# Performance work log

Measured on AMD Instinct MI355X. Metric: run time of the kernel, lower is better.

Reference implementation:

```python
import jax, jax.numpy as jnp
import numpy as np

B, S, D = 2, 2048, 2048
H, DK, DV, L = 16, 128, 128, 64


def setup_inputs() -> dict:
    key = jax.random.key(0)
    ks = jax.random.split(key, 12)
    s = lambda k, shape, fan_in: jax.random.normal(k, shape, jnp.float32) / np.sqrt(fan_in)
    return {
        "queries": jax.random.normal(ks[0], (B, S, D), jnp.float32),
        "keys": jax.random.normal(ks[1], (B, S, D), jnp.float32),
        "values": jax.random.normal(ks[2], (B, S, D), jnp.float32),
        "Wq": s(ks[3], (D, H * DK), D), "bq": jnp.zeros((H * DK,), jnp.float32),
        "Wlk": s(ks[4], (D, H * L), D), "blk": jnp.zeros((H * L,), jnp.float32),
        "Wlv": s(ks[5], (D, H * L), D), "blv": jnp.zeros((H * L,), jnp.float32),
        "Wkr": s(ks[6], (L, DK), L),
        "Wvr": s(ks[7], (L, DV), L),
        "Wout": s(ks[8], (H * DV, D), H * DV), "bout": jnp.zeros((D,), jnp.float32),
    }


def reference(queries, keys, values, Wq, bq, Wlk, blk, Wlv, blv, Wkr, Wvr, Wout, bout):
    b, sq, _ = queries.shape
    sk = keys.shape[1]
    # projections -> [b, h, s, d]
    q = (queries @ Wq + bq).reshape(b, sq, H, DK).transpose(0, 2, 1, 3)
    lk = (keys @ Wlk + blk).reshape(b, sk, H, L).transpose(0, 2, 1, 3)
    lv = (values @ Wlv + blv).reshape(b, sk, H, L).transpose(0, 2, 1, 3)
    k = lk @ Wkr  # [b,h,sk,DK] latent -> key reconstruction
    v = lv @ Wvr  # [b,h,sk,DV]
    scores = jnp.einsum('bhqd,bhkd->bhqk', q, k) / np.sqrt(DK).astype(np.float32)
    causal = jnp.triu(jnp.ones((sq, sk), dtype=bool), k=1)
    scores = jnp.where(causal, -jnp.inf, scores)
    attn = jax.nn.softmax(scores, axis=-1)
    out = jnp.einsum('bhqk,bhkd->bhqd', attn, v)
    out = out.transpose(0, 2, 1, 3).reshape(b, sq, H * DV)
    return out @ Wout + bout
```

## Files before the change

### kernel.cpp

```cpp
#include <hip/hip_runtime.h>
#include <cstdint>
#include <cstddef>

typedef _Float16 f16;
typedef __attribute__((ext_vector_type(8))) _Float16 f16x8;
typedef __attribute__((ext_vector_type(4))) _Float16 f16x4;
typedef __attribute__((ext_vector_type(4))) float f32x4;

constexpr int kB  = 2;
constexpr int kS  = 2048;
constexpr int kD  = 2048;
constexpr int kH  = 16;
constexpr int kL  = 64;
constexpr int kHL = kH * kL;
constexpr int kBS = kB * kS;

__device__ __forceinline__ void load_lds16(const void* g, void* l) {
  __builtin_amdgcn_global_load_lds((const __attribute__((address_space(1))) void*)g,
                                   (__attribute__((address_space(3))) void*)l, 16, 0, 0);
}

__device__ __forceinline__ f32x4 mfma16(f16x8 a, f16x8 b, f32x4 c) {
  return __builtin_amdgcn_mfma_f32_16x16x32_f16(a, b, c, 0, 0, 0);
}


__global__ void cast4(const float* __restrict__ a, const float* __restrict__ b,
                      const float* __restrict__ c, const float* __restrict__ d,
                      f16* __restrict__ oa, f16* __restrict__ ob,
                      f16* __restrict__ oc, f16* __restrict__ od) {
  const int z = blockIdx.z;
  int i = blockIdx.x * 256 + threadIdx.x;
  if (z == 3 && i >= kD * kD / 4) return;
  const float* in = z == 0 ? a : z == 1 ? b : z == 2 ? c : d;
  f16* out = z == 0 ? oa : z == 1 ? ob : z == 2 ? oc : od;
  float4 f = ((const float4*)in)[i];
  f16x4 o; o[0] = (f16)f.x; o[1] = (f16)f.y; o[2] = (f16)f.z; o[3] = (f16)f.w;
  ((f16x4*)out)[i] = o;
}

__device__ __forceinline__ void transpose_body(const float* __restrict__ in,
                                               f16* __restrict__ out, int R, int C) {
  const int r0 = blockIdx.y * 64, c0 = blockIdx.x * 64;
  __shared__ float tile[64][65];
  const int t = threadIdx.x;
  const int cc = t & 63, rr = t >> 6;
#pragma unroll
  for (int p = 0; p < 16; p++) {
    int r = p * 4 + rr;
    tile[r][cc] = in[(size_t)(r0 + r) * C + c0 + cc];
  }
  __syncthreads();
#pragma unroll
  for (int p = 0; p < 16; p++) {
    int c = p * 4 + rr;
    out[(size_t)(c0 + c) * R + r0 + cc] = (f16)tile[cc][c];
  }
}

__global__ __launch_bounds__(256) void transpose3(const float* __restrict__ Wlk,
                                                  const float* __restrict__ Wlv,
                                                  const float* __restrict__ Wout,
                                                  f16* __restrict__ Wlkt,
                                                  f16* __restrict__ Wlvt,
                                                  f16* __restrict__ WoutT) {
  const int z = blockIdx.z;
  if (z < 2 && blockIdx.x >= 16) return;
  if (z == 0) transpose_body(Wlk, Wlkt, 2048, 1024);
  else if (z == 1) transpose_body(Wlv, Wlvt, 2048, 1024);
  else transpose_body(Wout, WoutT, 2048, 2048);
}

__global__ void fold_bq(const float* __restrict__ bq, const float* __restrict__ Wkr,
                        float* __restrict__ bql) {
  int hl = blockIdx.x * 256 + threadIdx.x;
  if (hl >= kHL) return;
  int h = hl >> 6, l = hl & 63;
  float s = 0.f;
  for (int c = 0; c < 128; c++) s += bq[h * 128 + c] * Wkr[l * 128 + c];
  bql[hl] = s;
}

__global__ __launch_bounds__(256) void fold2(const float* __restrict__ Wkr,
                                             const float* __restrict__ Wvr,
                                             const f16* __restrict__ Wq16,
                                             const f16* __restrict__ WoutT,
                                             f16* __restrict__ Wqlt,
                                             f16* __restrict__ W2t) {
  __shared__ f16 sA[64 * 136];
  __shared__ f16 sB[128 * 128];
  const int z = blockIdx.z;
  const int h = blockIdx.y;
  const int d0 = blockIdx.x * 128;
  const float* Wsm = z ? Wvr : Wkr;
  const f16* Bsrc = (z ? WoutT : Wq16) + h * 128;
  const int tid = threadIdx.x;
  const int w = tid >> 6, lane = tid & 63;
  const int quad = lane >> 4, l16 = lane & 15;

#pragma unroll
  for (int it = 0; it < 8; it++) {
    int i = it * 256 + tid;
    float4 f = ((const float4*)Wsm)[i];
    int e = i * 4, r = e >> 7, c = e & 127;
    f16x4 o; o[0] = (f16)f.x; o[1] = (f16)f.y; o[2] = (f16)f.z; o[3] = (f16)f.w;
    *(f16x4*)&sA[r * 136 + c] = o;
  }
#pragma unroll
  for (int c = 0; c < 8; c++) {
    int rbase = w * 32 + c * 4;
    load_lds16(Bsrc + (size_t)(d0 + rbase + (lane >> 4)) * 2048 + (lane & 15) * 8,
               &sB[rbase * 128]);
  }
  __syncthreads();

  if (z == 0) {
    f32x4 acc[4][2];
    for (int mt = 0; mt < 4; mt++)
      for (int nt = 0; nt < 2; nt++) acc[mt][nt] = (f32x4){0.f, 0.f, 0.f, 0.f};
#pragma unroll
    for (int ks = 0; ks < 4; ks++) {
      f16x8 af[4], bf[2];
#pragma unroll
      for (int mt = 0; mt < 4; mt++)
        af[mt] = *(const f16x8*)&sA[(mt * 16 + l16) * 136 + ks * 32 + quad * 8];
#pragma unroll
      for (int nt = 0; nt < 2; nt++)
        bf[nt] = *(const f16x8*)&sB[(w * 32 + nt * 16 + l16) * 128 + ks * 32 + quad * 8];
#pragma unroll
      for (int mt = 0; mt < 4; mt++)
#pragma unroll
        for (int nt = 0; nt < 2; nt++) acc[mt][nt] = mfma16(af[mt], bf[nt], acc[mt][nt]);
    }
#pragma unroll
    for (int mt = 0; mt < 4; mt++)
#pragma unroll
      for (int nt = 0; nt < 2; nt++)
#pragma unroll
        for (int r = 0; r < 4; r++) {
          int row = mt * 16 + quad * 4 + r;
          int col = d0 + w * 32 + nt * 16 + l16;
          Wqlt[(size_t)(h * 64 + row) * 2048 + col] = (f16)acc[mt][nt][r];
        }
  } else {
    f32x4 acc[2][4];
    for (int mt = 0; mt < 2; mt++)
      for (int nt = 0; nt < 4; nt++) acc[mt][nt] = (f32x4){0.f, 0.f, 0.f, 0.f};
#pragma unroll
    for (int ks = 0; ks < 4; ks++) {
      f16x8 af[2], bf[4];
#pragma unroll
      for (int mt = 0; mt < 2; mt++)
        af[mt] = *(const f16x8*)&sB[(w * 32 + mt * 16 + l16) * 128 + ks * 32 + quad * 8];
#pragma unroll
      for (int nt = 0; nt < 4; nt++)
        bf[nt] = *(const f16x8*)&sA[(nt * 16 + l16) * 136 + ks * 32 + quad * 8];
#pragma unroll
      for (int mt = 0; mt < 2; mt++)
#pragma unroll
        for (int nt = 0; nt < 4; nt++) acc[mt][nt] = mfma16(af[mt], bf[nt], acc[mt][nt]);
    }
#pragma unroll
    for (int mt = 0; mt < 2; mt++)
#pragma unroll
      for (int nt = 0; nt < 4; nt++)
#pragma unroll
        for (int r = 0; r < 4; r++) {
          int row = d0 + w * 32 + mt * 16 + quad * 4 + r;
          int col = nt * 16 + l16;
          W2t[(size_t)row * 1024 + h * 64 + col] = (f16)acc[mt][nt][r];
        }
  }
}

template <typename OutT, bool HAS_BIAS>
__device__ __forceinline__ void gemm_body(const f16* __restrict__ A, const f16* __restrict__ Bt,
                                          const float* __restrict__ bias, OutT* __restrict__ C,
                                          int N, int K) {
  __shared__ f16 sA[128 * 64];
  __shared__ f16 sB[128 * 64];
  const int tid = threadIdx.x;
  const int w = tid >> 6, lane = tid & 63;
  const int quad = lane >> 4, l16 = lane & 15;
  const int wm = w >> 1, wn = w & 1;
  const int m0 = blockIdx.y * 128, n0 = blockIdx.x * 128;
  const int rowA = lane >> 3;
  const int colSw = (((lane & 7) ^ (lane >> 3)) << 3) ;
  const int sw0 = ((quad ^ (l16 & 7)) << 3);
  const int sw1 = (((4 + quad) ^ (l16 & 7)) << 3);

  f32x4 acc[4][4];
  for (int i = 0; i < 4; i++)
    for (int j = 0; j < 4; j++) acc[i][j] = (f32x4){0.f, 0.f, 0.f, 0.f};

  for (int k0 = 0; k0 < K; k0 += 64) {
    __syncthreads();
#pragma unroll
    for (int c = 0; c < 4; c++) {
      int rl = w * 32 + c * 8;
      load_lds16(A + (size_t)(m0 + rl + rowA) * K + k0 + colSw, &sA[rl * 64]);
      load_lds16(Bt + (size_t)(n0 + rl + rowA) * K + k0 + colSw, &sB[rl * 64]);
    }
    __syncthreads();
#pragma unroll
    for (int ks = 0; ks < 2; ks++) {
      const int sw = ks ? sw1 : sw0;
      f16x8 af[4], bfr[4];
#pragma unroll
      for (int mt = 0; mt < 4; mt++)
        af[mt] = *(const f16x8*)&sA[(wm * 64 + mt * 16 + l16) * 64 + sw];
#pragma unroll
      for (int nt = 0; nt < 4; nt++)
        bfr[nt] = *(const f16x8*)&sB[(wn * 64 + nt * 16 + l16) * 64 + sw];
#pragma unroll
      for (int mt = 0; mt < 4; mt++) {
#pragma unroll
        for (int nt = 0; nt < 4; nt++)
          acc[mt][nt] = mfma16(af[mt], bfr[nt], acc[mt][nt]);
      }
    }
  }
#pragma unroll
  for (int mt = 0; mt < 4; mt++) {
#pragma unroll
    for (int nt = 0; nt < 4; nt++) {
      int col = n0 + wn * 64 + nt * 16 + l16;
      float bv = HAS_BIAS ? bias[col] : 0.f;
#pragma unroll
      for (int r = 0; r < 4; r++) {
        int row = m0 + wm * 64 + mt * 16 + quad * 4 + r;
        C[(size_t)row * N + col] = (OutT)(acc[mt][nt][r] + bv);
      }
    }
  }
}

__global__ __launch_bounds__(256) void gemm3_f16(
    const f16* __restrict__ A0, const f16* __restrict__ A1, const f16* __restrict__ A2,
    const f16* __restrict__ B0, const f16* __restrict__ B1, const f16* __restrict__ B2,
    const float* __restrict__ c0, const float* __restrict__ c1, const float* __restrict__ c2,
    f16* __restrict__ C0, f16* __restrict__ C1, f16* __restrict__ C2, int N, int K) {
  const f16* A = blockIdx.z == 0 ? A0 : blockIdx.z == 1 ? A1 : A2;
  const f16* Bt = blockIdx.z == 0 ? B0 : blockIdx.z == 1 ? B1 : B2;
  const float* bias = blockIdx.z == 0 ? c0 : blockIdx.z == 1 ? c1 : c2;
  f16* C = blockIdx.z == 0 ? C0 : blockIdx.z == 1 ? C1 : C2;
  gemm_body<f16, true>(A, Bt, bias, C, N, K);
}

__global__ __launch_bounds__(256) void gemm_f32(const f16* __restrict__ A,
                                                const f16* __restrict__ Bt,
                                                const float* __restrict__ bias,
                                                float* __restrict__ C, int N, int K) {
  gemm_body<float, true>(A, Bt, bias, C, N, K);
}

__global__ __launch_bounds__(256) void transpose_lv(const f16* __restrict__ LV,
                                                    f16* __restrict__ LVt) {
  const int bh = blockIdx.y, b = bh >> 4, h = bh & 15;
  const int s0 = blockIdx.x * 64;
  __shared__ f16 tile[64][65];
  const int t = threadIdx.x;
  const int c0 = t & 63, r0 = t >> 6;
#pragma unroll
  for (int r = 0; r < 16; r++) {
    int s = r * 4 + r0;
    tile[s][c0] = LV[(size_t)(b * kS + s0 + s) * kHL + h * kL + c0];
  }
  __syncthreads();
#pragma unroll
  for (int r = 0; r < 16; r++) {
    int vl = r * 4 + r0;
    LVt[((size_t)bh * kL + vl) * kS + s0 + c0] = tile[c0][vl];
  }
}

__global__ __launch_bounds__(256) void attn(const f16* __restrict__ Qlat,
                                            const f16* __restrict__ LK,
                                            const f16* __restrict__ LVt,
                                            f16* __restrict__ Ctx) {
  const int bh = blockIdx.y, b = bh >> 4, h = bh & 15;
  const int pair = blockIdx.x;
  const int tid = threadIdx.x;
  const int w = tid >> 6, lane = tid & 63;
  const int quad = lane >> 4, l16 = lane & 15;

  __shared__ f16 sK[2][64 * 64];
  __shared__ f16 sV[2][64 * 64];
  __shared__ f16 sP[4][16 * 72];

  const f16* qbase = Qlat + (size_t)b * kS * kHL + h * kL;
  const f16* kbase = LK + (size_t)b * kS * kHL + h * kL;
  const f16* vbase = LVt + (size_t)bh * kL * kS;

  const float cscale = 0.08838834764831845f * 1.4426950408889634f;
  const int rowA = lane >> 3;
  const int colSw = (((lane & 7) ^ (lane >> 3)) << 3);
  const int sw0 = ((quad ^ (l16 & 7)) << 3);
  const int sw1 = (((4 + quad) ^ (l16 & 7)) << 3);

  for (int which = 0; which < 2; which++) {
    const int t = which ? (31 - pair) : pair;
    const int q0 = t * 64;
    const int qrow = q0 + w * 16 + l16;
    const int qg = qrow;
    const int ntile = t + 1;

    f16x8 aq[2];
#pragma unroll
    for (int ks = 0; ks < 2; ks++)
      aq[ks] = *(const f16x8*)(qbase + (size_t)qrow * kHL + ks * 32 + quad * 8);

    f32x4 acc[4];
    for (int nt = 0; nt < 4; nt++) acc[nt] = (f32x4){0.f, 0.f, 0.f, 0.f};
    float m_s = -3.0e38f;
    float l_part = 0.f;

    __syncthreads();
    {
      const int rl = w * 16;
      load_lds16(kbase + (size_t)(rl + rowA) * kHL + colSw, &sK[0][rl * 64]);
      load_lds16(vbase + (size_t)(rl + rowA) * kS + colSw, &sV[0][rl * 64]);
      load_lds16(kbase + (size_t)(rl + 8 + rowA) * kHL + colSw, &sK[0][(rl + 8) * 64]);
      load_lds16(vbase + (size_t)(rl + 8 + rowA) * kS + colSw, &sV[0][(rl + 8) * 64]);
    }
    int cur = 0;

    for (int it = 0; it < ntile; ++it) {
      const int kv0 = it * 64;
      __syncthreads();

      if (it + 1 < ntile) {
        const int nkv = kv0 + 64;
        f16* dK = &sK[cur ^ 1][0];
        f16* dV = &sV[cur ^ 1][0];
        const int rl = w * 16;
        load_lds16(kbase + (size_t)(nkv + rl + rowA) * kHL + colSw, dK + rl * 64);
        load_lds16(vbase + (size_t)(rl + rowA) * kS + nkv + colSw, dV + rl * 64);
        load_lds16(kbase + (size_t)(nkv + rl + 8 + rowA) * kHL + colSw, dK + (rl + 8) * 64);
        load_lds16(vbase + (size_t)(rl + 8 + rowA) * kS + nkv + colSw, dV + (rl + 8) * 64);
      }
      const f16* sKc = &sK[cur][0];
      const f16* sVc = &sV[cur][0];

      f32x4 sc[4];
      for (int nt = 0; nt < 4; nt++) sc[nt] = (f32x4){0.f, 0.f, 0.f, 0.f};
#pragma unroll
      for (int ks = 0; ks < 2; ks++) {
        const int sw = ks ? sw1 : sw0;
        f16x8 bk[4];
#pragma unroll
        for (int nt = 0; nt < 4; nt++)
          bk[nt] = *(const f16x8*)&sKc[(nt * 16 + l16) * 64 + sw];
#pragma unroll
        for (int nt = 0; nt < 4; nt++) sc[nt] = mfma16(bk[nt], aq[ks], sc[nt]);
      }

      if (kv0 == q0) {
#pragma unroll
        for (int nt = 0; nt < 4; nt++) {
#pragma unroll
          for (int r = 0; r < 4; r++) {
            int kvg = kv0 + nt * 16 + quad * 4 + r;
            if (kvg > qg) sc[nt][r] = -1.0e30f;
          }
        }
      }

      float tm = -3.0e38f;
#pragma unroll
      for (int nt = 0; nt < 4; nt++)
        tm = fmaxf(tm, fmaxf(fmaxf(sc[nt][0], sc[nt][1]), fmaxf(sc[nt][2], sc[nt][3])));
      tm = fmaxf(tm, __shfl_xor(tm, 16));
      tm = fmaxf(tm, __shfl_xor(tm, 32));
      const float tms = tm * cscale;

      if (!__all(tms <= m_s)) {
        const float mnew = fmaxf(m_s, tms);
        const float alpha = __builtin_amdgcn_exp2f(m_s - mnew);
        m_s = mnew;
        l_part *= alpha;
        float ar[4];
#pragma unroll
        for (int r = 0; r < 4; r++) ar[r] = __shfl(alpha, quad * 4 + r);
#pragma unroll
        for (int nt = 0; nt < 4; nt++)
#pragma unroll
          for (int r = 0; r < 4; r++) acc[nt][r] *= ar[r];
      }

      float ps = 0.f;
#pragma unroll
      for (int nt = 0; nt < 4; nt++) {
        f16x4 pk;
#pragma unroll
        for (int r = 0; r < 4; r++) {
          float p = __builtin_amdgcn_exp2f(__builtin_fmaf(sc[nt][r], cscale, -m_s));
          ps += p;
          pk[r] = (f16)p;
        }
        *(f16x4*)&sP[w][l16 * 72 + nt * 16 + quad * 4] = pk;
      }
      l_part += ps;

#pragma unroll
      for (int ks = 0; ks < 2; ks++) {
        const int sw = ks ? sw1 : sw0;
        f16x8 ap = *(const f16x8*)&sP[w][l16 * 72 + ks * 32 + quad * 8];
        f16x8 bv[4];
#pragma unroll
        for (int nt = 0; nt < 4; nt++)
          bv[nt] = *(const f16x8*)&sVc[(nt * 16 + l16) * 64 + sw];
#pragma unroll
        for (int nt = 0; nt < 4; nt++) acc[nt] = mfma16(ap, bv[nt], acc[nt]);
      }
      cur ^= 1;
    }

    float lfull = l_part;
    lfull += __shfl_xor(lfull, 16);
    lfull += __shfl_xor(lfull, 32);
    float inv[4];
#pragma unroll
    for (int r = 0; r < 4; r++) inv[r] = 1.f / __shfl(lfull, quad * 4 + r);
#pragma unroll
    for (int r = 0; r < 4; r++) {
      int qout = q0 + w * 16 + quad * 4 + r;
      size_t base = (size_t)(b * kS + qout) * kHL + h * kL;
#pragma unroll
      for (int nt = 0; nt < 4; nt++)
        Ctx[base + nt * 16 + l16] = (f16)(acc[nt][r] * inv[r]);
    }
  }
}

extern "C" void kernel_launch(void* const* d_in, const int* in_sizes, int n_in,
                              void* d_out, int out_size, void* d_ws, size_t ws_size,
                              hipStream_t stream) {
  (void)in_sizes; (void)n_in; (void)out_size; (void)ws_size;
  const float* queries = (const float*)d_in[0];
  const float* keys    = (const float*)d_in[1];
  const float* values  = (const float*)d_in[2];
  const float* Wq      = (const float*)d_in[3];
  const float* bq      = (const float*)d_in[4];
  const float* Wlk     = (const float*)d_in[5];
  const float* blk     = (const float*)d_in[6];
  const float* Wlv     = (const float*)d_in[7];
  const float* blv     = (const float*)d_in[8];
  const float* Wkr     = (const float*)d_in[9];
  const float* Wvr     = (const float*)d_in[10];
  const float* Wout    = (const float*)d_in[11];
  const float* bout    = (const float*)d_in[12];

  char* ws = (char*)d_ws;
  size_t off = 0;
  auto alloc = [&](size_t bytes) {
    void* p = ws + off;
    off += (bytes + 255) & ~(size_t)255;
    return p;
  };
  f16* qb    = (f16*)alloc((size_t)kBS * kD * 2);
  f16* kb    = (f16*)alloc((size_t)kBS * kD * 2);
  f16* vb    = (f16*)alloc((size_t)kBS * kD * 2);
  f16* Wqlt  = (f16*)alloc((size_t)kHL * kD * 2);
  f16* Wlkt  = (f16*)alloc((size_t)kHL * kD * 2);
  f16* Wlvt  = (f16*)alloc((size_t)kHL * kD * 2);
  f16* W2t   = (f16*)alloc((size_t)kD * kHL * 2);
  float* bql = (float*)alloc(kHL * 4);
  f16* Qlat  = (f16*)alloc((size_t)kBS * kHL * 2);
  f16* LKb   = (f16*)alloc((size_t)kBS * kHL * 2);
  f16* LVb   = (f16*)alloc((size_t)kBS * kHL * 2);
  f16* Wq16  = Qlat;
  f16* WoutT = LKb;
  f16* LVtb = qb;
  f16* Ctx  = kb;

  const int n4 = kBS * kD / 4;
  cast4<<<dim3(n4 / 256, 1, 4), 256, 0, stream>>>(queries, keys, values, Wq, qb, kb, vb, Wq16);
  transpose3<<<dim3(32, 32, 3), 256, 0, stream>>>(Wlk, Wlv, Wout, Wlkt, Wlvt, WoutT);
  fold_bq<<<kHL / 256, 256, 0, stream>>>(bq, Wkr, bql);
  fold2<<<dim3(16, 16, 2), 256, 0, stream>>>(Wkr, Wvr, Wq16, WoutT, Wqlt, W2t);

  gemm3_f16<<<dim3(kHL / 128, kBS / 128, 3), 256, 0, stream>>>(
      qb, kb, vb, Wqlt, Wlkt, Wlvt, bql, blk, blv, Qlat, LKb, LVb, kHL, kD);

  transpose_lv<<<dim3(kS / 64, kB * kH), 256, 0, stream>>>(LVb, LVtb);
  attn<<<dim3(16, kB * kH), 256, 0, stream>>>(Qlat, LKb, LVtb, Ctx);
  gemm_f32<<<dim3(kD / 128, kBS / 128), 256, 0, stream>>>(Ctx, W2t, bout, (float*)d_out, kD, kHL);
}
```

Before: 371.9 us.

## Double-buffer GEMM LDS tiles and add XCD-aware block swizzle

The shared GEMM body now keeps two LDS buffers for the A and B tiles. It prefetches the next K-slice with async global-to-LDS loads while the MFMAs run on the current one, which leaves a single barrier per iteration. The projection and output GEMM kernels also remap block indices so that neighbouring tiles land on the same XCD, aiming for better L2 reuse. This doubles LDS use per block, which can lower occupancy. There is no explicit wait on the async loads beyond the barrier, which relies on the compiler inserting a vmcnt wait.

After: 362.5 us. 2.5% less time.

```diff
diff --git a/kernel.cpp b/kernel.cpp
--- a/kernel.cpp
+++ b/kernel.cpp
@@ -176,16 +176,15 @@
 template <typename OutT, bool HAS_BIAS>
 __device__ __forceinline__ void gemm_body(const f16* __restrict__ A, const f16* __restrict__ Bt,
                                           const float* __restrict__ bias, OutT* __restrict__ C,
-                                          int N, int K) {
-  __shared__ f16 sA[128 * 64];
-  __shared__ f16 sB[128 * 64];
+                                          int N, int K, int m0, int n0) {
+  __shared__ f16 sA[2][128 * 64];
+  __shared__ f16 sB[2][128 * 64];
   const int tid = threadIdx.x;
   const int w = tid >> 6, lane = tid & 63;
   const int quad = lane >> 4, l16 = lane & 15;
   const int wm = w >> 1, wn = w & 1;
-  const int m0 = blockIdx.y * 128, n0 = blockIdx.x * 128;
   const int rowA = lane >> 3;
-  const int colSw = (((lane & 7) ^ (lane >> 3)) << 3) ;
+  const int colSw = (((lane & 7) ^ (lane >> 3)) << 3);
   const int sw0 = ((quad ^ (l16 & 7)) << 3);
   const int sw1 = (((4 + quad) ^ (l16 & 7)) << 3);
 
@@ -193,25 +192,37 @@
   for (int i = 0; i < 4; i++)
     for (int j = 0; j < 4; j++) acc[i][j] = (f32x4){0.f, 0.f, 0.f, 0.f};
 
+#pragma unroll
+  for (int c = 0; c < 4; c++) {
+    int rl = w * 32 + c * 8;
+    load_lds16(A + (size_t)(m0 + rl + rowA) * K + colSw, &sA[0][rl * 64]);
+    load_lds16(Bt + (size_t)(n0 + rl + rowA) * K + colSw, &sB[0][rl * 64]);
+  }
+  int cur = 0;
+
   for (int k0 = 0; k0 < K; k0 += 64) {
     __syncthreads();
-#pragma unroll
-    for (int c = 0; c < 4; c++) {
-      int rl = w * 32 + c * 8;
-      load_lds16(A + (size_t)(m0 + rl + rowA) * K + k0 + colSw, &sA[rl * 64]);
-      load_lds16(Bt + (size_t)(n0 + rl + rowA) * K + k0 + colSw, &sB[rl * 64]);
-    }
-    __syncthreads();
+    if (k0 + 64 < K) {
+      const int nk = k0 + 64;
+#pragma unroll
+      for (int c = 0; c < 4; c++) {
+        int rl = w * 32 + c * 8;
+        load_lds16(A + (size_t)(m0 + rl + rowA) * K + nk + colSw, &sA[cur ^ 1][rl * 64]);
+        load_lds16(Bt + (size_t)(n0 + rl + rowA) * K + nk + colSw, &sB[cur ^ 1][rl * 64]);
+      }
+    }
+    const f16* sAc = &sA[cur][0];
+    const f16* sBc = &sB[cur][0];
 #pragma unroll
     for (int ks = 0; ks < 2; ks++) {
       const int sw = ks ? sw1 : sw0;
       f16x8 af[4], bfr[4];
 #pragma unroll
       for (int mt = 0; mt < 4; mt++)
-        af[mt] = *(const f16x8*)&sA[(wm * 64 + mt * 16 + l16) * 64 + sw];
+        af[mt] = *(const f16x8*)&sAc[(wm * 64 + mt * 16 + l16) * 64 + sw];
 #pragma unroll
       for (int nt = 0; nt < 4; nt++)
-        bfr[nt] = *(const f16x8*)&sB[(wn * 64 + nt * 16 + l16) * 64 + sw];
+        bfr[nt] = *(const f16x8*)&sBc[(wn * 64 + nt * 16 + l16) * 64 + sw];
 #pragma unroll
       for (int mt = 0; mt < 4; mt++) {
 #pragma unroll
@@ -219,6 +230,7 @@
           acc[mt][nt] = mfma16(af[mt], bfr[nt], acc[mt][nt]);
       }
     }
+    cur ^= 1;
   }
 #pragma unroll
   for (int mt = 0; mt < 4; mt++) {
@@ -233,6 +245,11 @@
       }
     }
   }
+}
+
+__device__ __forceinline__ int xcd_swizzle(int flat, int nwg) {
+  const int cpx = nwg >> 3;
+  return (flat & 7) * cpx + (flat >> 3);
 }
 
 __global__ __launch_bounds__(256) void gemm3_f16(
@@ -244,14 +261,18 @@
   const f16* Bt = blockIdx.z == 0 ? B0 : blockIdx.z == 1 ? B1 : B2;
   const float* bias = blockIdx.z == 0 ? c0 : blockIdx.z == 1 ? c1 : c2;
   f16* C = blockIdx.z == 0 ? C0 : blockIdx.z == 1 ? C1 : C2;
-  gemm_body<f16, true>(A, Bt, bias, C, N, K);
+  const int nx = gridDim.x;
+  int swz = xcd_swizzle(blockIdx.y * nx + blockIdx.x, nx * gridDim.y);
+  gemm_body<f16, true>(A, Bt, bias, C, N, K, (swz / nx) * 128, (swz % nx) * 128);
 }
 
 __global__ __launch_bounds__(256) void gemm_f32(const f16* __restrict__ A,
                                                 const f16* __restrict__ Bt,
                                                 const float* __restrict__ bias,
                                                 float* __restrict__ C, int N, int K) {
-  gemm_body<float, true>(A, Bt, bias, C, N, K);
+  const int nx = gridDim.x;
+  int swz = xcd_swizzle(blockIdx.y * nx + blockIdx.x, nx * gridDim.y);
+  gemm_body<float, true>(A, Bt, bias, C, N, K, (swz / nx) * 128, (swz % nx) * 128);
 }
 
 __global__ __launch_bounds__(256) void transpose_lv(const f16* __restrict__ LV,
```

## Prefetch GEMM tiles through registers and add XCD-aware block swizzle

Applied to the files above, without the earlier changes.

Replaces the direct global-to-LDS loads in the shared GEMM body with a register-staged software pipeline. The next K tile is loaded into registers while MFMAs run on the current LDS tile, then written to swizzled LDS between barriers. It also remaps the flat block index so that consecutive tiles land on the same XCD, which should improve L2 reuse. The price is more VGPR pressure, explicit barriers and waitcnt, and the assumption that the block count divides by 8.

Result: faster. 359.1 us (-3.4%).

```diff
diff --git a/kernel.cpp b/kernel.cpp
--- a/kernel.cpp
+++ b/kernel.cpp
@@ -23,7 +23,6 @@
 __device__ __forceinline__ f32x4 mfma16(f16x8 a, f16x8 b, f32x4 c) {
   return __builtin_amdgcn_mfma_f32_16x16x32_f16(a, b, c, 0, 0, 0);
 }
-
 
 __global__ void cast4(const float* __restrict__ a, const float* __restrict__ b,
                       const float* __restrict__ c, const float* __restrict__ d,
@@ -176,32 +175,59 @@
 template <typename OutT, bool HAS_BIAS>
 __device__ __forceinline__ void gemm_body(const f16* __restrict__ A, const f16* __restrict__ Bt,
                                           const float* __restrict__ bias, OutT* __restrict__ C,
-                                          int N, int K) {
+                                          int N, int K, int m0, int n0) {
   __shared__ f16 sA[128 * 64];
   __shared__ f16 sB[128 * 64];
   const int tid = threadIdx.x;
   const int w = tid >> 6, lane = tid & 63;
   const int quad = lane >> 4, l16 = lane & 15;
   const int wm = w >> 1, wn = w & 1;
-  const int m0 = blockIdx.y * 128, n0 = blockIdx.x * 128;
-  const int rowA = lane >> 3;
-  const int colSw = (((lane & 7) ^ (lane >> 3)) << 3) ;
   const int sw0 = ((quad ^ (l16 & 7)) << 3);
   const int sw1 = (((4 + quad) ^ (l16 & 7)) << 3);
+
+  const int srow = tid >> 3;
+  const int schunk = tid & 7;
+  const f16* aG = A + (size_t)(m0 + srow) * K + schunk * 8;
+  const f16* bG = Bt + (size_t)(n0 + srow) * K + schunk * 8;
+  const int wxor = (schunk ^ (srow & 7)) * 8;
+  int wof0 = (srow + 0) * 64 + wxor;
+  int wof1 = (srow + 32) * 64 + wxor;
+  int wof2 = (srow + 64) * 64 + wxor;
+  int wof3 = (srow + 96) * 64 + wxor;
+
+  float4 ra0, ra1, ra2, ra3, rb0, rb1, rb2, rb3;
+
+#define LOAD_TILE(k0)                                                            \
+  do {                                                                           \
+    ra0 = *(const float4*)(aG + (k0));                                           \
+    ra1 = *(const float4*)(aG + (size_t)32 * K + (k0));                          \
+    ra2 = *(const float4*)(aG + (size_t)64 * K + (k0));                          \
+    ra3 = *(const float4*)(aG + (size_t)96 * K + (k0));                          \
+    rb0 = *(const float4*)(bG + (k0));                                           \
+    rb1 = *(const float4*)(bG + (size_t)32 * K + (k0));                          \
+    rb2 = *(const float4*)(bG + (size_t)64 * K + (k0));                          \
+    rb3 = *(const float4*)(bG + (size_t)96 * K + (k0));                          \
+  } while (0)
+
+#define WRITE_TILE()                                                             \
+  do {                                                                           \
+    *(float4*)&sA[wof0] = ra0; *(float4*)&sA[wof1] = ra1;                        \
+    *(float4*)&sA[wof2] = ra2; *(float4*)&sA[wof3] = ra3;                        \
+    *(float4*)&sB[wof0] = rb0; *(float4*)&sB[wof1] = rb1;                        \
+    *(float4*)&sB[wof2] = rb2; *(float4*)&sB[wof3] = rb3;                        \
+  } while (0)
 
   f32x4 acc[4][4];
   for (int i = 0; i < 4; i++)
     for (int j = 0; j < 4; j++) acc[i][j] = (f32x4){0.f, 0.f, 0.f, 0.f};
 
-  for (int k0 = 0; k0 < K; k0 += 64) {
-    __syncthreads();
-#pragma unroll
-    for (int c = 0; c < 4; c++) {
-      int rl = w * 32 + c * 8;
-      load_lds16(A + (size_t)(m0 + rl + rowA) * K + k0 + colSw, &sA[rl * 64]);
-      load_lds16(Bt + (size_t)(n0 + rl + rowA) * K + k0 + colSw, &sB[rl * 64]);
-    }
-    __syncthreads();
+  const int nt = K >> 6;
+  LOAD_TILE(0);
+  WRITE_TILE();
+  LOAD_TILE(64);
+  __syncthreads();
+
+  for (int t = 0; t < nt; ++t) {
 #pragma unroll
     for (int ks = 0; ks < 2; ks++) {
       const int sw = ks ? sw1 : sw0;
@@ -210,29 +236,48 @@
       for (int mt = 0; mt < 4; mt++)
         af[mt] = *(const f16x8*)&sA[(wm * 64 + mt * 16 + l16) * 64 + sw];
 #pragma unroll
-      for (int nt = 0; nt < 4; nt++)
-        bfr[nt] = *(const f16x8*)&sB[(wn * 64 + nt * 16 + l16) * 64 + sw];
+      for (int ntf = 0; ntf < 4; ntf++)
+        bfr[ntf] = *(const f16x8*)&sB[(wn * 64 + ntf * 16 + l16) * 64 + sw];
 #pragma unroll
       for (int mt = 0; mt < 4; mt++) {
 #pragma unroll
-        for (int nt = 0; nt < 4; nt++)
-          acc[mt][nt] = mfma16(af[mt], bfr[nt], acc[mt][nt]);
-      }
-    }
-  }
+        for (int ntf = 0; ntf < 4; ntf++)
+          acc[mt][ntf] = mfma16(af[mt], bfr[ntf], acc[mt][ntf]);
+      }
+    }
+    if (t + 1 < nt) {
+      __builtin_amdgcn_sched_barrier(0);
+      __builtin_amdgcn_s_barrier();
+      __builtin_amdgcn_sched_barrier(0);
+      WRITE_TILE();
+      if (t + 2 < nt) LOAD_TILE((t + 2) << 6);
+      asm volatile("s_waitcnt lgkmcnt(0)" ::: "memory");
+      __builtin_amdgcn_sched_barrier(0);
+      __builtin_amdgcn_s_barrier();
+      __builtin_amdgcn_sched_barrier(0);
+    }
+  }
+#undef LOAD_TILE
+#undef WRITE_TILE
+
 #pragma unroll
   for (int mt = 0; mt < 4; mt++) {
 #pragma unroll
-    for (int nt = 0; nt < 4; nt++) {
-      int col = n0 + wn * 64 + nt * 16 + l16;
+    for (int ntf = 0; ntf < 4; ntf++) {
+      int col = n0 + wn * 64 + ntf * 16 + l16;
       float bv = HAS_BIAS ? bias[col] : 0.f;
 #pragma unroll
       for (int r = 0; r < 4; r++) {
         int row = m0 + wm * 64 + mt * 16 + quad * 4 + r;
-        C[(size_t)row * N + col] = (OutT)(acc[mt][nt][r] + bv);
-      }
-    }
-  }
+        C[(size_t)row * N + col] = (OutT)(acc[mt][ntf][r] + bv);
+      }
+    }
+  }
+}
+
+__device__ __forceinline__ int xcd_swizzle(int flat, int nwg) {
+  const int cpx = nwg >> 3;
+  return (flat & 7) * cpx + (flat >> 3);
 }
 
 __global__ __launch_bounds__(256) void gemm3_f16(
@@ -244,14 +289,18 @@
   const f16* Bt = blockIdx.z == 0 ? B0 : blockIdx.z == 1 ? B1 : B2;
   const float* bias = blockIdx.z == 0 ? c0 : blockIdx.z == 1 ? c1 : c2;
   f16* C = blockIdx.z == 0 ? C0 : blockIdx.z == 1 ? C1 : C2;
-  gemm_body<f16, true>(A, Bt, bias, C, N, K);
+  const int nx = gridDim.x;
+  int swz = xcd_swizzle(blockIdx.y * nx + blockIdx.x, nx * gridDim.y);
+  gemm_body<f16, true>(A, Bt, bias, C, N, K, (swz / nx) * 128, (swz % nx) * 128);
 }
 
 __global__ __launch_bounds__(256) void gemm_f32(const f16* __restrict__ A,
                                                 const f16* __restrict__ Bt,
                                                 const float* __restrict__ bias,
                                                 float* __restrict__ C, int N, int K) {
-  gemm_body<float, true>(A, Bt, bias, C, N, K);
+  const int nx = gridDim.x;
+  int swz = xcd_swizzle(blockIdx.y * nx + blockIdx.x, nx * gridDim.y);
+  gemm_body<float, true>(A, Bt, bias, C, N, K, (swz / nx) * 128, (swz % nx) * 128);
 }
 
 __global__ __launch_bounds__(256) void transpose_lv(const f16* __restrict__ LV,
```
